# Performance work log

Hardware: AMD Instinct MI355X
Metric: run time of the kernel (lower is better)

Reference implementation:

```python
import jax, jax.numpy as jnp
import numpy as np
from jax import lax

DIM = 64
NUM_EXPERTS = 6
TOP_K = 2
B, H, W = 8, 128, 128
DN = ('NCHW', 'OIHW', 'NCHW')


def setup_inputs() -> dict:
    key = jax.random.key(0)
    ks = jax.random.split(key, 8)
    s_in = 1.0 / np.sqrt(DIM * 9)
    s_r = 1.0 / np.sqrt(DIM)
    return {
        'x': jax.random.normal(ks[0], (B, DIM, H, W), jnp.float32),
        'router_w': jax.random.normal(ks[1], (NUM_EXPERTS, DIM), jnp.float32) * s_r,
        'router_b': jnp.zeros((NUM_EXPERTS,), jnp.float32),
        'expert_bias': jnp.zeros((NUM_EXPERTS,), jnp.float32),
        'w1': jax.random.normal(ks[2], (NUM_EXPERTS, DIM, DIM, 3, 3), jnp.float32) * s_in,
        'b1': jnp.zeros((NUM_EXPERTS, DIM), jnp.float32),
        'w2': jax.random.normal(ks[3], (NUM_EXPERTS, DIM, DIM, 3, 3), jnp.float32) * s_in,
        'b2': jnp.zeros((NUM_EXPERTS, DIM), jnp.float32),
    }


def reference(x, router_w, router_b, expert_bias, w1, b1, w2, b2):
    # ---- router: global avg pool -> linear -> clamp -> +bias -> softmax ----
    pooled = x.mean(axis=(2, 3))                               # [B, C]
    logits = pooled @ router_w.T + router_b                    # [B, E]
    logits = jnp.clip(logits, -10.0, 10.0) + expert_bias[None, :]
    probs = jnp.clip(jax.nn.softmax(logits, axis=1), 1e-6, 1.0)
    top_v, top_i = lax.top_k(probs, TOP_K)                     # [B, K]
    top_v = top_v / (top_v.sum(axis=1, keepdims=True) + 1e-8)
    # per-sample combine weight for each expert: sum of top-k probs routed to it
    w_be = (jax.nn.one_hot(top_i, NUM_EXPERTS, dtype=x.dtype) * top_v[..., None]).sum(axis=1)  # [B, E]

    # ---- experts: Conv3x3 -> GELU -> Conv3x3, vmapped over expert dim ----
    def expert(w1e, b1e, w2e, b2e):
        h = lax.conv_general_dilated(x, w1e, (1, 1), 'SAME', dimension_numbers=DN)
        h = jax.nn.gelu(h + b1e[None, :, None, None])
        h = lax.conv_general_dilated(h, w2e, (1, 1), 'SAME', dimension_numbers=DN)
        return h + b2e[None, :, None, None]

    ys = jax.vmap(expert)(w1, b1, w2, b2)                      # [E, B, C, H, W]
    out = jnp.einsum('be,ebchw->bchw', w_be, ys)
    return out, jnp.zeros((), x.dtype)
```

## Files before the change

### kernel.cpp

```cpp
#include <hip/hip_runtime.h>
#include <hip/hip_bf16.h>
#include <cstdint>

typedef __attribute__((ext_vector_type(8))) short sh8;
typedef __attribute__((ext_vector_type(16))) float f32x16;
typedef unsigned short ushort_t;

#define HH 128
#define WW 128
#define HWSZ (HH*WW)
#define PW 130
#define PW64 (PW*64)
#define IMGSZ ((size_t)PW*PW*64)
#define WBEXP 36864

#define TR 8
#define SROWS 10
#define SCOLS 34
#define ASTR (SCOLS*128)
#define ACHUNKS (SROWS*SCOLS*8)

__device__ __forceinline__ float gelu_tanh(float x) {
    float u = 0.7978845608028654f * (x + 0.044715f * x * x * x);
    return 0.5f * x * (1.0f + tanhf(u));
}
__device__ __forceinline__ ushort_t f2b(float f) {
    __hip_bfloat16 h = __float2bfloat16(f);
    return *reinterpret_cast<ushort_t*>(&h);
}
__device__ __forceinline__ f32x16 mfma_bf16(sh8 a, sh8 b, f32x16 c) {
    return __builtin_amdgcn_mfma_f32_32x32x16_bf16(a, b, c, 0, 0, 0);
}

__device__ __forceinline__ void stage_tile(const ushort_t* __restrict__ imgRow,
                                           char* smem, int w0, int tid) {
#pragma unroll
    for (int it = 0; it < 11; ++it) {
        int idx = tid + it * 256;
        if (idx < ACHUNKS) {
            int row = idx / (SCOLS * 8);
            int rem = idx - row * (SCOLS * 8);
            int col = rem >> 3, ch = rem & 7;
            uint4 v = *reinterpret_cast<const uint4*>(
                imgRow + (size_t)row * PW64 + (size_t)(w0 + col) * 64 + ch * 8);
            int byt = row * ASTR + ((col * 128 + ch * 16) ^ ((col & 7) << 4));
            *reinterpret_cast<uint4*>(smem + byt) = v;
        }
    }
}

__global__ __launch_bounds__(64) void router_kernel(const float* __restrict__ pooled,
                                                    const float* __restrict__ rw,
                                                    const float* __restrict__ rb,
                                                    const float* __restrict__ eb,
                                                    const float* __restrict__ b2,
                                                    int* __restrict__ topi,
                                                    float* __restrict__ topw,
                                                    float* __restrict__ bsum,
                                                    float* __restrict__ outz) {
    __shared__ int sti[16];
    __shared__ float stw[16];
    int b = threadIdx.x;
    if (b == 8) outz[(size_t)8 * 64 * HWSZ] = 0.f;
    if (b < 8) {
        float lg[6];
        for (int e = 0; e < 6; ++e) {
            float s = 0.f;
            for (int c = 0; c < 64; ++c) s += pooled[b * 64 + c] * rw[e * 64 + c];
            s = s * (1.0f / (float)HWSZ) + rb[e];
            lg[e] = fminf(fmaxf(s, -10.f), 10.f) + eb[e];
        }
        float m = lg[0];
        for (int e = 1; e < 6; ++e) m = fmaxf(m, lg[e]);
        float den = 0.f, pr[6];
        for (int e = 0; e < 6; ++e) { pr[e] = expf(lg[e] - m); den += pr[e]; }
        float inv = 1.0f / den;
        for (int e = 0; e < 6; ++e) pr[e] = fminf(fmaxf(pr[e] * inv, 1e-6f), 1.0f);
        int i0 = 0; float v0 = pr[0];
        for (int e = 1; e < 6; ++e) if (pr[e] > v0) { v0 = pr[e]; i0 = e; }
        int i1 = -1; float v1 = -1.f;
        for (int e = 0; e < 6; ++e) { if (e == i0) continue; if (pr[e] > v1) { v1 = pr[e]; i1 = e; } }
        float s2 = v0 + v1 + 1e-8f;
        topi[b * 2 + 0] = i0; topi[b * 2 + 1] = i1;
        topw[b * 2 + 0] = v0 / s2; topw[b * 2 + 1] = v1 / s2;
        sti[b * 2 + 0] = i0; sti[b * 2 + 1] = i1;
        stw[b * 2 + 0] = v0 / s2; stw[b * 2 + 1] = v1 / s2;
    }
    __syncthreads();
    for (int i = threadIdx.x; i < 512; i += 64) {
        int bb = i >> 6, c = i & 63;
        bsum[i] = stw[bb * 2] * b2[sti[bb * 2] * 64 + c] +
                  stw[bb * 2 + 1] * b2[sti[bb * 2 + 1] * 64 + c];
    }
}

__global__ __launch_bounds__(256) void convx_kernel(const float* __restrict__ x,
                                                    ushort_t* __restrict__ xp,
                                                    float* __restrict__ pooled) {
    __shared__ ushort_t lt[128][72];
    int b = blockIdx.x >> 7, h = blockIdx.x & 127;
    int tid = threadIdx.x;
#pragma unroll
    for (int k = 0; k < 8; ++k) {
        int idx = tid + k * 256;
        int ci = idx >> 5, wg = idx & 31;
        float4 v = *reinterpret_cast<const float4*>(
            x + ((size_t)b * 64 + ci) * HWSZ + (size_t)h * WW + wg * 4);
        lt[wg * 4 + 0][ci] = f2b(v.x);
        lt[wg * 4 + 1][ci] = f2b(v.y);
        lt[wg * 4 + 2][ci] = f2b(v.z);
        lt[wg * 4 + 3][ci] = f2b(v.w);
        float s4 = (v.x + v.y) + (v.z + v.w);
#pragma unroll
        for (int m = 16; m > 0; m >>= 1) s4 += __shfl_xor(s4, m, 64);
        if ((tid & 31) == 0) atomicAdd(pooled + b * 64 + ci, s4);
    }
    __syncthreads();
    int w = tid >> 1, half = tid & 1;
    const int4* src = reinterpret_cast<const int4*>(&lt[w][half * 32]);
    int4 a0 = src[0], a1 = src[1], a2 = src[2], a3 = src[3];
    int4* dst = reinterpret_cast<int4*>(
        xp + (((size_t)b * PW + (h + 1)) * PW + (w + 1)) * 64 + half * 32);
    dst[0] = a0; dst[1] = a1; dst[2] = a2; dst[3] = a3;
}

__global__ __launch_bounds__(256) void convw1_kernel(const float* __restrict__ w1,
                                                     ushort_t* __restrict__ wb1f) {
    int blk = blockIdx.x;
    int e = blk / 9, t = blk - e * 9;
    for (int idx = threadIdx.x; idx < 4096; idx += 256) {
        int kc = idx >> 10, n = (idx >> 9) & 1, l = (idx >> 3) & 63, j = idx & 7;
        int co = n * 32 + (l & 31);
        int ci = kc * 16 + (l >> 5) * 8 + j;
        wb1f[(size_t)e * WBEXP + t * 4096 + idx] =
            f2b(w1[(((size_t)e * 64 + co) * 64 + ci) * 9 + t]);
    }
}

__global__ __launch_bounds__(256) void convw2_kernel(const float* __restrict__ w2,
                                                     const int* __restrict__ topi,
                                                     const float* __restrict__ topw,
                                                     ushort_t* __restrict__ wb2f) {
    int blk = blockIdx.x;
    int bs = blk / 9, t = blk - bs * 9;
    int e = topi[bs];
    float cw = topw[bs];
    for (int idx = threadIdx.x; idx < 4096; idx += 256) {
        int kc = idx >> 10, n = (idx >> 9) & 1, l = (idx >> 3) & 63, j = idx & 7;
        int co = n * 32 + (l & 31);
        int ci = kc * 16 + (l >> 5) * 8 + j;
        wb2f[(size_t)bs * WBEXP + t * 4096 + idx] =
            f2b(cw * w2[(((size_t)e * 64 + co) * 64 + ci) * 9 + t]);
    }
}

__global__ __launch_bounds__(256) void halo_kernel(ushort_t* __restrict__ xp,
                                                   ushort_t* __restrict__ hp) {
    int img = blockIdx.x;
    ushort_t* p = (img < 8) ? (xp + (size_t)img * IMGSZ) : (hp + (size_t)(img - 8) * IMGSZ);
    int tid = threadIdx.x;
    int4 z = make_int4(0, 0, 0, 0);
    for (int i = tid; i < 1040; i += 256) {
        reinterpret_cast<int4*>(p)[i] = z;
        reinterpret_cast<int4*>(p + (size_t)129 * PW64)[i] = z;
    }
    for (int i = tid; i < 128 * 8; i += 256) {
        int row = 1 + (i >> 3), j = i & 7;
        reinterpret_cast<int4*>(p + (size_t)row * PW64)[j] = z;
        reinterpret_cast<int4*>(p + ((size_t)row * PW + 129) * 64)[j] = z;
    }
}

__global__ __launch_bounds__(256) void conv1_mfma(const ushort_t* __restrict__ xp,
                                                  const ushort_t* __restrict__ wb1f,
                                                  const float* __restrict__ b1,
                                                  const int* __restrict__ topi,
                                                  ushort_t* __restrict__ hp,
                                                  int nslots, int slot0) {
    __shared__ uint4 smem4[ACHUNKS];
    char* smem = (char*)smem4;
    const int z = blockIdx.z;
    const int b = z / nslots, sl = z - b * nslots, s = slot0 + sl;
    const int e = topi[b * 2 + s];
    const int tid = threadIdx.x, l = tid & 63, wid = tid >> 6;
    const int l31 = l & 31, lh = l >> 5;
    const int ht = blockIdx.x >> 2, wt = blockIdx.x & 3;
    const int h0 = ht * TR, w0 = wt * 32;
    const int r0 = wid * 2;

    stage_tile(xp + (size_t)b * IMGSZ + (size_t)h0 * PW64, smem, w0, tid);
    __syncthreads();

    const ushort_t* wB = wb1f + (size_t)e * WBEXP + l * 8;
    f32x16 acc00, acc01, acc10, acc11;
#pragma unroll
    for (int k2 = 0; k2 < 16; ++k2) { acc00[k2] = 0.f; acc01[k2] = 0.f; acc10[k2] = 0.f; acc11[k2] = 0.f; }

#pragma unroll
    for (int dr = 0; dr < 3; ++dr) {
#pragma unroll
        for (int dc = 0; dc < 3; ++dc) {
            const int t = dr * 3 + dc;
            const int col = dc + l31;
            const int swz = (col & 7) << 4;
#pragma unroll
            for (int kc = 0; kc < 4; ++kc) {
                const int cb = (col * 128 + kc * 32 + lh * 16) ^ swz;
                sh8 a0 = *reinterpret_cast<const sh8*>(smem + (r0 + dr) * ASTR + cb);
                sh8 a1 = *reinterpret_cast<const sh8*>(smem + (r0 + dr + 1) * ASTR + cb);
                sh8 b0 = *reinterpret_cast<const sh8*>(wB + (t * 4 + kc) * 1024);
                sh8 b1 = *reinterpret_cast<const sh8*>(wB + (t * 4 + kc) * 1024 + 512);
                acc00 = mfma_bf16(a0, b0, acc00);
                acc01 = mfma_bf16(a0, b1, acc01);
                acc10 = mfma_bf16(a1, b0, acc10);
                acc11 = mfma_bf16(a1, b1, acc11);
            }
        }
    }

    const float bv0 = b1[e * 64 + l31];
    const float bv1 = b1[e * 64 + 32 + l31];
    const size_t base =
        (((size_t)(sl * 8 + b) * PW + (h0 + r0 + 1)) * PW + (w0 + 1)) * 64 + l31;
#pragma unroll
    for (int i = 0; i < 2; ++i) {
#pragma unroll
        for (int n = 0; n < 2; ++n) {
            f32x16 a = (i == 0) ? (n == 0 ? acc00 : acc01) : (n == 0 ? acc10 : acc11);
            const float bv = n ? bv1 : bv0;
            const size_t ob = base + (size_t)i * PW64 + n * 32;
#pragma unroll
            for (int r = 0; r < 16; ++r) {
                int px = (r & 3) + 8 * (r >> 2) + 4 * lh;
                hp[ob + (size_t)px * 64] = f2b(gelu_tanh(a[r] + bv));
            }
        }
    }
}

template <int NS>
__global__ __launch_bounds__(256) void conv2_mfma(const ushort_t* __restrict__ hp,
                                                  const ushort_t* __restrict__ wb2f,
                                                  const float* __restrict__ bsum,
                                                  float* __restrict__ outF,
                                                  int s0, int addmode) {
    __shared__ uint4 smem4[ACHUNKS];
    char* smem = (char*)smem4;
    const int b = blockIdx.z;
    const int tid = threadIdx.x, l = tid & 63, wid = tid >> 6;
    const int l31 = l & 31, lh = l >> 5;
    const int ht = blockIdx.x >> 2, wt = blockIdx.x & 3;
    const int h0 = ht * TR, w0 = wt * 32;
    const int r0 = wid * 2;

    f32x16 acc00, acc01, acc10, acc11;
#pragma unroll
    for (int k2 = 0; k2 < 16; ++k2) { acc00[k2] = 0.f; acc01[k2] = 0.f; acc10[k2] = 0.f; acc11[k2] = 0.f; }

    for (int si = 0; si < NS; ++si) {
        __syncthreads();
        stage_tile(hp + (size_t)(si * 8 + b) * IMGSZ + (size_t)h0 * PW64, smem, w0, tid);
        __syncthreads();

        const ushort_t* wB = wb2f + (size_t)(b * 2 + s0 + si) * WBEXP + l * 8;
#pragma unroll
        for (int dr = 0; dr < 3; ++dr) {
#pragma unroll
            for (int dc = 0; dc < 3; ++dc) {
                const int t = dr * 3 + dc;
                const int col = dc + l31;
                const int swz = (col & 7) << 4;
#pragma unroll
                for (int kc = 0; kc < 4; ++kc) {
                    const int cb = (col * 128 + kc * 32 + lh * 16) ^ swz;
                    sh8 a0 = *reinterpret_cast<const sh8*>(smem + (r0 + dr) * ASTR + cb);
                    sh8 a1 = *reinterpret_cast<const sh8*>(smem + (r0 + dr + 1) * ASTR + cb);
                    sh8 b0 = *reinterpret_cast<const sh8*>(wB + (t * 4 + kc) * 1024);
                    sh8 b1 = *reinterpret_cast<const sh8*>(wB + (t * 4 + kc) * 1024 + 512);
                    acc00 = mfma_bf16(a0, b0, acc00);
                    acc01 = mfma_bf16(a0, b1, acc01);
                    acc10 = mfma_bf16(a1, b0, acc10);
                    acc11 = mfma_bf16(a1, b1, acc11);
                }
            }
        }
    }

    __syncthreads();
    float* lt = (float*)smem4;
    const float bq0 = addmode ? 0.f : bsum[b * 64 + l31];
    const float bq1 = addmode ? 0.f : bsum[b * 64 + 32 + l31];
#pragma unroll
    for (int i = 0; i < 2; ++i) {
        const int h = h0 + r0 + i;
#pragma unroll
        for (int n = 0; n < 2; ++n) {
            f32x16 a = (i == 0) ? (n == 0 ? acc00 : acc01) : (n == 0 ? acc10 : acc11);
            const float bq = n ? bq1 : bq0;
#pragma unroll
            for (int r = 0; r < 16; ++r) {
                int px = (r & 3) + 8 * (r >> 2) + 4 * lh;
                lt[wid * 1056 + px * 33 + l31] = a[r] + bq;
            }
            const int q = lh, co = l31;
            const size_t ob = ((size_t)(b * 64 + n * 32 + co)) * HWSZ +
                              (size_t)h * WW + w0 + q * 16;
#pragma unroll
            for (int v = 0; v < 4; ++v) {
                float o0 = lt[wid * 1056 + (q * 16 + v * 4 + 0) * 33 + co];
                float o1 = lt[wid * 1056 + (q * 16 + v * 4 + 1) * 33 + co];
                float o2 = lt[wid * 1056 + (q * 16 + v * 4 + 2) * 33 + co];
                float o3 = lt[wid * 1056 + (q * 16 + v * 4 + 3) * 33 + co];
                float4* dst = reinterpret_cast<float4*>(outF + ob + v * 4);
                if (addmode) {
                    float4 pv = *dst;
                    o0 += pv.x; o1 += pv.y; o2 += pv.z; o3 += pv.w;
                }
                float4 o; o.x = o0; o.y = o1; o.z = o2; o.w = o3;
                *dst = o;
            }
        }
    }
}

extern "C" void kernel_launch(void* const* d_in, const int* in_sizes, int n_in,
                              void* d_out, int out_size, void* d_ws, size_t ws_size,
                              hipStream_t stream) {
    const float* x  = (const float*)d_in[0];
    const float* rw = (const float*)d_in[1];
    const float* rb = (const float*)d_in[2];
    const float* eb = (const float*)d_in[3];
    const float* w1 = (const float*)d_in[4];
    const float* b1 = (const float*)d_in[5];
    const float* w2 = (const float*)d_in[6];
    const float* b2 = (const float*)d_in[7];
    float* out = (float*)d_out;

    char* ws = (char*)d_ws;
    float*    pooled = (float*)(ws + 0);
    int*      topi   = (int*)(ws + 2048);
    float*    topw   = (float*)(ws + 2112);
    float*    bsum   = (float*)(ws + 2176);
    ushort_t* wb1f   = (ushort_t*)(ws + 4352);
    ushort_t* wb2f   = (ushort_t*)(ws + 446720);
    ushort_t* xp     = (ushort_t*)(ws + 1626368);
    ushort_t* hp     = (ushort_t*)(ws + 18931968);

    const bool two = ws_size >= 53543168ull;

    hipMemsetAsync(pooled, 0, 512 * sizeof(float), stream);
    hipLaunchKernelGGL(convx_kernel, dim3(1024), dim3(256), 0, stream, x, xp, pooled);
    hipLaunchKernelGGL(router_kernel, dim3(1), dim3(64), 0, stream,
                       pooled, rw, rb, eb, b2, topi, topw, bsum, out);
    hipLaunchKernelGGL(convw1_kernel, dim3(54), dim3(256), 0, stream, w1, wb1f);
    hipLaunchKernelGGL(convw2_kernel, dim3(144), dim3(256), 0, stream, w2, topi, topw, wb2f);
    hipLaunchKernelGGL(halo_kernel, dim3(two ? 24 : 16), dim3(256), 0, stream, xp, hp);

    if (two) {
        hipLaunchKernelGGL(conv1_mfma, dim3(64, 1, 16), dim3(256), 0, stream,
                           xp, wb1f, b1, topi, hp, 2, 0);
        hipLaunchKernelGGL((conv2_mfma<2>), dim3(64, 1, 8), dim3(256), 0, stream,
                           hp, wb2f, bsum, out, 0, 0);
    } else {
        hipLaunchKernelGGL(conv1_mfma, dim3(64, 1, 8), dim3(256), 0, stream,
                           xp, wb1f, b1, topi, hp, 1, 0);
        hipLaunchKernelGGL((conv2_mfma<1>), dim3(64, 1, 8), dim3(256), 0, stream,
                           hp, wb2f, bsum, out, 0, 0);
        hipLaunchKernelGGL(conv1_mfma, dim3(64, 1, 8), dim3(256), 0, stream,
                           xp, wb1f, b1, topi, hp, 1, 1);
        hipLaunchKernelGGL((conv2_mfma<1>), dim3(64, 1, 8), dim3(256), 0, stream,
                           hp, wb2f, bsum, out, 1, 1);
    }
}
```

Measured before the change: 251.7 us.

## Use direct global-to-LDS loads, merge prep kernels, retile conv2 with double-buffered slots

Tile staging switches to global_load_lds, which copies straight into shared memory without going through registers, and moves the XOR swizzle onto the source address. The three weight-convert and halo kernels become one prep kernel to cut launch overhead. Conv1's epilogue writes packed bf16 vectors instead of scalar stores. Conv2 now uses 4-row tiles on a grid of twice as many blocks and prefetches the second slot's tile into a separate buffer while the first is computed. The risks are lower arithmetic intensity per conv2 block and more dependence on compiler scheduling around the sched_barrier hints.

Result: faster. 213.6 us (-15.2%).

```diff
diff --git a/kernel.cpp b/kernel.cpp
--- a/kernel.cpp
+++ b/kernel.cpp
@@ -14,11 +14,17 @@
 #define IMGSZ ((size_t)PW*PW*64)
 #define WBEXP 36864
 
-#define TR 8
-#define SROWS 10
 #define SCOLS 34
-#define ASTR (SCOLS*128)
-#define ACHUNKS (SROWS*SCOLS*8)
+#define ROWB (SCOLS*128)
+#define TR1 8
+#define SR1 10
+#define CH1 (SR1*SCOLS*8)
+#define TR2 4
+#define SR2 6
+#define CH2 (SR2*SCOLS*8)
+
+typedef __attribute__((address_space(1))) const void gvoid_t;
+typedef __attribute__((address_space(3))) void lvoid_t;
 
 __device__ __forceinline__ float gelu_tanh(float x) {
     float u = 0.7978845608028654f * (x + 0.044715f * x * x * x);
@@ -28,23 +34,27 @@
     __hip_bfloat16 h = __float2bfloat16(f);
     return *reinterpret_cast<ushort_t*>(&h);
 }
+__device__ __forceinline__ unsigned pack2(float a, float b) {
+    return (unsigned)f2b(a) | ((unsigned)f2b(b) << 16);
+}
 __device__ __forceinline__ f32x16 mfma_bf16(sh8 a, sh8 b, f32x16 c) {
     return __builtin_amdgcn_mfma_f32_32x32x16_bf16(a, b, c, 0, 0, 0);
 }
 
-__device__ __forceinline__ void stage_tile(const ushort_t* __restrict__ imgRow,
-                                           char* smem, int w0, int tid) {
-#pragma unroll
-    for (int it = 0; it < 11; ++it) {
+template <int NCH>
+__device__ __forceinline__ void stage_gll(const ushort_t* __restrict__ imgRow,
+                                          char* smem, int w0, int tid) {
+#pragma unroll
+    for (int it = 0; it < (NCH + 255) / 256; ++it) {
         int idx = tid + it * 256;
-        if (idx < ACHUNKS) {
+        if ((NCH & 255) == 0 || idx < NCH) {
             int row = idx / (SCOLS * 8);
             int rem = idx - row * (SCOLS * 8);
-            int col = rem >> 3, ch = rem & 7;
-            uint4 v = *reinterpret_cast<const uint4*>(
-                imgRow + (size_t)row * PW64 + (size_t)(w0 + col) * 64 + ch * 8);
-            int byt = row * ASTR + ((col * 128 + ch * 16) ^ ((col & 7) << 4));
-            *reinterpret_cast<uint4*>(smem + byt) = v;
+            int col = rem >> 3;
+            int ch  = (rem & 7) ^ (col & 7);
+            const ushort_t* src = imgRow + (size_t)row * PW64 + (size_t)(w0 + col) * 64 + ch * 8;
+            __builtin_amdgcn_global_load_lds((gvoid_t*)src, (lvoid_t*)(smem + idx * 16),
+                                             16, 0, 0);
         }
     }
 }
@@ -124,50 +134,71 @@
     dst[0] = a0; dst[1] = a1; dst[2] = a2; dst[3] = a3;
 }
 
-__global__ __launch_bounds__(256) void convw1_kernel(const float* __restrict__ w1,
-                                                     ushort_t* __restrict__ wb1f) {
+__global__ __launch_bounds__(256) void prep_kernel(const float* __restrict__ w1,
+                                                   const float* __restrict__ w2,
+                                                   const int* __restrict__ topi,
+                                                   const float* __restrict__ topw,
+                                                   ushort_t* __restrict__ wb1f,
+                                                   ushort_t* __restrict__ wb2f,
+                                                   ushort_t* __restrict__ xp,
+                                                   ushort_t* __restrict__ hp) {
     int blk = blockIdx.x;
-    int e = blk / 9, t = blk - e * 9;
-    for (int idx = threadIdx.x; idx < 4096; idx += 256) {
-        int kc = idx >> 10, n = (idx >> 9) & 1, l = (idx >> 3) & 63, j = idx & 7;
-        int co = n * 32 + (l & 31);
-        int ci = kc * 16 + (l >> 5) * 8 + j;
-        wb1f[(size_t)e * WBEXP + t * 4096 + idx] =
-            f2b(w1[(((size_t)e * 64 + co) * 64 + ci) * 9 + t]);
-    }
-}
-
-__global__ __launch_bounds__(256) void convw2_kernel(const float* __restrict__ w2,
-                                                     const int* __restrict__ topi,
-                                                     const float* __restrict__ topw,
-                                                     ushort_t* __restrict__ wb2f) {
-    int blk = blockIdx.x;
-    int bs = blk / 9, t = blk - bs * 9;
-    int e = topi[bs];
-    float cw = topw[bs];
-    for (int idx = threadIdx.x; idx < 4096; idx += 256) {
-        int kc = idx >> 10, n = (idx >> 9) & 1, l = (idx >> 3) & 63, j = idx & 7;
-        int co = n * 32 + (l & 31);
-        int ci = kc * 16 + (l >> 5) * 8 + j;
-        wb2f[(size_t)bs * WBEXP + t * 4096 + idx] =
-            f2b(cw * w2[(((size_t)e * 64 + co) * 64 + ci) * 9 + t]);
-    }
-}
-
-__global__ __launch_bounds__(256) void halo_kernel(ushort_t* __restrict__ xp,
-                                                   ushort_t* __restrict__ hp) {
-    int img = blockIdx.x;
-    ushort_t* p = (img < 8) ? (xp + (size_t)img * IMGSZ) : (hp + (size_t)(img - 8) * IMGSZ);
     int tid = threadIdx.x;
-    int4 z = make_int4(0, 0, 0, 0);
-    for (int i = tid; i < 1040; i += 256) {
-        reinterpret_cast<int4*>(p)[i] = z;
-        reinterpret_cast<int4*>(p + (size_t)129 * PW64)[i] = z;
-    }
-    for (int i = tid; i < 128 * 8; i += 256) {
-        int row = 1 + (i >> 3), j = i & 7;
-        reinterpret_cast<int4*>(p + (size_t)row * PW64)[j] = z;
-        reinterpret_cast<int4*>(p + ((size_t)row * PW + 129) * 64)[j] = z;
+    if (blk < 54) {
+        int e = blk / 9, t = blk - e * 9;
+        for (int idx = tid; idx < 4096; idx += 256) {
+            int kc = idx >> 10, n = (idx >> 9) & 1, l = (idx >> 3) & 63, j = idx & 7;
+            int co = n * 32 + (l & 31);
+            int ci = kc * 16 + (l >> 5) * 8 + j;
+            wb1f[(size_t)e * WBEXP + t * 4096 + idx] =
+                f2b(w1[(((size_t)e * 64 + co) * 64 + ci) * 9 + t]);
+        }
+    } else if (blk < 198) {
+        int q = blk - 54;
+        int bs = q / 9, t = q - bs * 9;
+        int e = topi[bs];
+        float cw = topw[bs];
+        for (int idx = tid; idx < 4096; idx += 256) {
+            int kc = idx >> 10, n = (idx >> 9) & 1, l = (idx >> 3) & 63, j = idx & 7;
+            int co = n * 32 + (l & 31);
+            int ci = kc * 16 + (l >> 5) * 8 + j;
+            wb2f[(size_t)bs * WBEXP + t * 4096 + idx] =
+                f2b(cw * w2[(((size_t)e * 64 + co) * 64 + ci) * 9 + t]);
+        }
+    } else {
+        int img = blk - 198;
+        ushort_t* p = (img < 8) ? (xp + (size_t)img * IMGSZ)
+                                : (hp + (size_t)(img - 8) * IMGSZ);
+        int4 z = make_int4(0, 0, 0, 0);
+        for (int i = tid; i < 1040; i += 256) {
+            reinterpret_cast<int4*>(p)[i] = z;
+            reinterpret_cast<int4*>(p + (size_t)129 * PW64)[i] = z;
+        }
+        for (int i = tid; i < 128 * 8; i += 256) {
+            int row = 1 + (i >> 3), j = i & 7;
+            reinterpret_cast<int4*>(p + (size_t)row * PW64)[j] = z;
+            reinterpret_cast<int4*>(p + ((size_t)row * PW + 129) * 64)[j] = z;
+        }
+    }
+}
+
+__device__ __forceinline__ void conv_phase1(const char* sm, const ushort_t* wt_,
+                                            int row, int l31, int lh,
+                                            f32x16& acc0, f32x16& acc1, int dc) {
+    sh8 wf[8];
+#pragma unroll
+    for (int kc = 0; kc < 4; ++kc) {
+        wf[kc * 2]     = *reinterpret_cast<const sh8*>(wt_ + kc * 1024);
+        wf[kc * 2 + 1] = *reinterpret_cast<const sh8*>(wt_ + kc * 1024 + 512);
+    }
+    __builtin_amdgcn_sched_barrier(0);
+    const int colb = (dc + l31) * 128;
+    const int swz = ((dc + l31) & 7) << 4;
+#pragma unroll
+    for (int kc = 0; kc < 4; ++kc) {
+        sh8 a = *reinterpret_cast<const sh8*>(sm + row * ROWB + ((colb + (kc * 2 + lh) * 16) ^ swz));
+        acc0 = mfma_bf16(wf[kc * 2], a, acc0);
+        acc1 = mfma_bf16(wf[kc * 2 + 1], a, acc1);
     }
 }
 
@@ -177,62 +208,72 @@
                                                   const int* __restrict__ topi,
                                                   ushort_t* __restrict__ hp,
                                                   int nslots, int slot0) {
-    __shared__ uint4 smem4[ACHUNKS];
-    char* smem = (char*)smem4;
+    __shared__ char smem[CH1 * 16];
     const int z = blockIdx.z;
     const int b = z / nslots, sl = z - b * nslots, s = slot0 + sl;
     const int e = topi[b * 2 + s];
     const int tid = threadIdx.x, l = tid & 63, wid = tid >> 6;
     const int l31 = l & 31, lh = l >> 5;
     const int ht = blockIdx.x >> 2, wt = blockIdx.x & 3;
-    const int h0 = ht * TR, w0 = wt * 32;
+    const int h0 = ht * TR1, w0 = wt * 32;
     const int r0 = wid * 2;
 
-    stage_tile(xp + (size_t)b * IMGSZ + (size_t)h0 * PW64, smem, w0, tid);
-    __syncthreads();
+    stage_gll<CH1>(xp + (size_t)b * IMGSZ + (size_t)h0 * PW64, smem, w0, tid);
 
     const ushort_t* wB = wb1f + (size_t)e * WBEXP + l * 8;
     f32x16 acc00, acc01, acc10, acc11;
 #pragma unroll
     for (int k2 = 0; k2 < 16; ++k2) { acc00[k2] = 0.f; acc01[k2] = 0.f; acc10[k2] = 0.f; acc11[k2] = 0.f; }
+    __syncthreads();
 
 #pragma unroll
     for (int dr = 0; dr < 3; ++dr) {
 #pragma unroll
         for (int dc = 0; dc < 3; ++dc) {
-            const int t = dr * 3 + dc;
-            const int col = dc + l31;
-            const int swz = (col & 7) << 4;
+            const ushort_t* wt_ = wB + (dr * 3 + dc) * 4096;
+            sh8 wf[8];
 #pragma unroll
             for (int kc = 0; kc < 4; ++kc) {
-                const int cb = (col * 128 + kc * 32 + lh * 16) ^ swz;
-                sh8 a0 = *reinterpret_cast<const sh8*>(smem + (r0 + dr) * ASTR + cb);
-                sh8 a1 = *reinterpret_cast<const sh8*>(smem + (r0 + dr + 1) * ASTR + cb);
-                sh8 b0 = *reinterpret_cast<const sh8*>(wB + (t * 4 + kc) * 1024);
-                sh8 b1 = *reinterpret_cast<const sh8*>(wB + (t * 4 + kc) * 1024 + 512);
-                acc00 = mfma_bf16(a0, b0, acc00);
-                acc01 = mfma_bf16(a0, b1, acc01);
-                acc10 = mfma_bf16(a1, b0, acc10);
-                acc11 = mfma_bf16(a1, b1, acc11);
+                wf[kc * 2]     = *reinterpret_cast<const sh8*>(wt_ + kc * 1024);
+                wf[kc * 2 + 1] = *reinterpret_cast<const sh8*>(wt_ + kc * 1024 + 512);
             }
-        }
-    }
-
-    const float bv0 = b1[e * 64 + l31];
-    const float bv1 = b1[e * 64 + 32 + l31];
-    const size_t base =
-        (((size_t)(sl * 8 + b) * PW + (h0 + r0 + 1)) * PW + (w0 + 1)) * 64 + l31;
+            __builtin_amdgcn_sched_barrier(0);
+            const int colb = (dc + l31) * 128;
+            const int swz = ((dc + l31) & 7) << 4;
+#pragma unroll
+            for (int kc = 0; kc < 4; ++kc) {
+                const int cb = (colb + (kc * 2 + lh) * 16) ^ swz;
+                sh8 a0 = *reinterpret_cast<const sh8*>(smem + (r0 + dr) * ROWB + cb);
+                sh8 a1 = *reinterpret_cast<const sh8*>(smem + (r0 + dr + 1) * ROWB + cb);
+                acc00 = mfma_bf16(wf[kc * 2], a0, acc00);
+                acc01 = mfma_bf16(wf[kc * 2 + 1], a0, acc01);
+                acc10 = mfma_bf16(wf[kc * 2], a1, acc10);
+                acc11 = mfma_bf16(wf[kc * 2 + 1], a1, acc11);
+            }
+        }
+    }
+
+    float4 bq[2][4];
+#pragma unroll
+    for (int n = 0; n < 2; ++n)
+#pragma unroll
+        for (int g = 0; g < 4; ++g)
+            bq[n][g] = *reinterpret_cast<const float4*>(b1 + e * 64 + n * 32 + g * 8 + 4 * lh);
+    const size_t pbase = (size_t)(sl * 8 + b) * IMGSZ +
+                         (size_t)(h0 + r0 + 1) * PW64 + (size_t)(w0 + l31 + 1) * 64;
 #pragma unroll
     for (int i = 0; i < 2; ++i) {
 #pragma unroll
         for (int n = 0; n < 2; ++n) {
             f32x16 a = (i == 0) ? (n == 0 ? acc00 : acc01) : (n == 0 ? acc10 : acc11);
-            const float bv = n ? bv1 : bv0;
-            const size_t ob = base + (size_t)i * PW64 + n * 32;
-#pragma unroll
-            for (int r = 0; r < 16; ++r) {
-                int px = (r & 3) + 8 * (r >> 2) + 4 * lh;
-                hp[ob + (size_t)px * 64] = f2b(gelu_tanh(a[r] + bv));
+#pragma unroll
+            for (int g = 0; g < 4; ++g) {
+                float v0 = gelu_tanh(a[g * 4 + 0] + bq[n][g].x);
+                float v1 = gelu_tanh(a[g * 4 + 1] + bq[n][g].y);
+                float v2 = gelu_tanh(a[g * 4 + 2] + bq[n][g].z);
+                float v3 = gelu_tanh(a[g * 4 + 3] + bq[n][g].w);
+                uint2 u; u.x = pack2(v0, v1); u.y = pack2(v2, v3);
+                *reinterpret_cast<uint2*>(hp + pbase + (size_t)i * PW64 + n * 32 + g * 8 + 4 * lh) = u;
             }
         }
     }
@@ -244,81 +285,77 @@
                                                   const float* __restrict__ bsum,
                                                   float* __restrict__ outF,
                                                   int s0, int addmode) {
-    __shared__ uint4 smem4[ACHUNKS];
-    char* smem = (char*)smem4;
+    __shared__ char smem[2][CH2 * 16];
     const int b = blockIdx.z;
     const int tid = threadIdx.x, l = tid & 63, wid = tid >> 6;
     const int l31 = l & 31, lh = l >> 5;
     const int ht = blockIdx.x >> 2, wt = blockIdx.x & 3;
-    const int h0 = ht * TR, w0 = wt * 32;
-    const int r0 = wid * 2;
-
-    f32x16 acc00, acc01, acc10, acc11;
-#pragma unroll
-    for (int k2 = 0; k2 < 16; ++k2) { acc00[k2] = 0.f; acc01[k2] = 0.f; acc10[k2] = 0.f; acc11[k2] = 0.f; }
-
-    for (int si = 0; si < NS; ++si) {
+    const int h0 = ht * TR2, w0 = wt * 32;
+    const int row0 = wid;
+
+    stage_gll<CH2>(hp + (size_t)b * IMGSZ + (size_t)h0 * PW64, smem[0], w0, tid);
+
+    f32x16 acc0, acc1;
+#pragma unroll
+    for (int k2 = 0; k2 < 16; ++k2) { acc0[k2] = 0.f; acc1[k2] = 0.f; }
+    __syncthreads();
+
+    if (NS == 2)
+        stage_gll<CH2>(hp + (size_t)(8 + b) * IMGSZ + (size_t)h0 * PW64, smem[1], w0, tid);
+
+    {
+        const ushort_t* wB = wb2f + (size_t)(b * 2 + s0) * WBEXP + l * 8;
+#pragma unroll
+        for (int dr = 0; dr < 3; ++dr)
+#pragma unroll
+            for (int dc = 0; dc < 3; ++dc)
+                conv_phase1(smem[0], wB + (dr * 3 + dc) * 4096, row0 + dr, l31, lh, acc0, acc1, dc);
+    }
+    if (NS == 2) {
         __syncthreads();
-        stage_tile(hp + (size_t)(si * 8 + b) * IMGSZ + (size_t)h0 * PW64, smem, w0, tid);
-        __syncthreads();
-
-        const ushort_t* wB = wb2f + (size_t)(b * 2 + s0 + si) * WBEXP + l * 8;
-#pragma unroll
-        for (int dr = 0; dr < 3; ++dr) {
-#pragma unroll
-            for (int dc = 0; dc < 3; ++dc) {
-                const int t = dr * 3 + dc;
-                const int col = dc + l31;
-                const int swz = (col & 7) << 4;
-#pragma unroll
-                for (int kc = 0; kc < 4; ++kc) {
-                    const int cb = (col * 128 + kc * 32 + lh * 16) ^ swz;
-                    sh8 a0 = *reinterpret_cast<const sh8*>(smem + (r0 + dr) * ASTR + cb);
-                    sh8 a1 = *reinterpret_cast<const sh8*>(smem + (r0 + dr + 1) * ASTR + cb);
-                    sh8 b0 = *reinterpret_cast<const sh8*>(wB + (t * 4 + kc) * 1024);
-                    sh8 b1 = *reinterpret_cast<const sh8*>(wB + (t * 4 + kc) * 1024 + 512);
-                    acc00 = mfma_bf16(a0, b0, acc00);
-                    acc01 = mfma_bf16(a0, b1, acc01);
-                    acc10 = mfma_bf16(a1, b0, acc10);
-                    acc11 = mfma_bf16(a1, b1, acc11);
-                }
+        const ushort_t* wB = wb2f + (size_t)(b * 2 + s0 + 1) * WBEXP + l * 8;
+#pragma unroll
+        for (int dr = 0; dr < 3; ++dr)
+#pragma unroll
+            for (int dc = 0; dc < 3; ++dc)
+                conv_phase1(smem[1], wB + (dr * 3 + dc) * 4096, row0 + dr, l31, lh, acc0, acc1, dc);
+    }
+
+    __syncthreads();
+    float* lt = reinterpret_cast<float*>(smem[0]) + wid * 1056;
+    float4 bq[2][4];
+#pragma unroll
+    for (int n = 0; n < 2; ++n)
+#pragma unroll
+        for (int g = 0; g < 4; ++g)
+            bq[n][g] = addmode ? make_float4(0.f, 0.f, 0.f, 0.f)
+                               : *reinterpret_cast<const float4*>(bsum + b * 64 + n * 32 + g * 8 + 4 * lh);
+    const int h = h0 + row0;
+#pragma unroll
+    for (int n = 0; n < 2; ++n) {
+        f32x16 a = n ? acc1 : acc0;
+#pragma unroll
+        for (int r = 0; r < 16; ++r) {
+            int co = (r & 3) + 8 * (r >> 2) + 4 * lh;
+            float bv = (r & 3) == 0 ? bq[n][r >> 2].x : (r & 3) == 1 ? bq[n][r >> 2].y
+                     : (r & 3) == 2 ? bq[n][r >> 2].z : bq[n][r >> 2].w;
+            lt[l31 * 33 + co] = a[r] + bv;
+        }
+        const int q = lh, co = l31;
+        const size_t ob = ((size_t)(b * 64 + n * 32 + co)) * HWSZ + (size_t)h * WW + w0 + q * 16;
+#pragma unroll
+        for (int v = 0; v < 4; ++v) {
+            float o0 = lt[(q * 16 + v * 4 + 0) * 33 + co];
+            float o1 = lt[(q * 16 + v * 4 + 1) * 33 + co];
+            float o2 = lt[(q * 16 + v * 4 + 2) * 33 + co];
+            float o3 = lt[(q * 16 + v * 4 + 3) * 33 + co];
+            float4* dst = reinterpret_cast<float4*>(outF + ob + v * 4);
+            if (addmode) {
+                float4 pv = *dst;
+                o0 += pv.x; o1 += pv.y; o2 += pv.z; o3 += pv.w;
             }
-        }
-    }
-
-    __syncthreads();
-    float* lt = (float*)smem4;
-    const float bq0 = addmode ? 0.f : bsum[b * 64 + l31];
-    const float bq1 = addmode ? 0.f : bsum[b * 64 + 32 + l31];
-#pragma unroll
-    for (int i = 0; i < 2; ++i) {
-        const int h = h0 + r0 + i;
-#pragma unroll
-        for (int n = 0; n < 2; ++n) {
-            f32x16 a = (i == 0) ? (n == 0 ? acc00 : acc01) : (n == 0 ? acc10 : acc11);
-            const float bq = n ? bq1 : bq0;
-#pragma unroll
-            for (int r = 0; r < 16; ++r) {
-                int px = (r & 3) + 8 * (r >> 2) + 4 * lh;
-                lt[wid * 1056 + px * 33 + l31] = a[r] + bq;
-            }
-            const int q = lh, co = l31;
-            const size_t ob = ((size_t)(b * 64 + n * 32 + co)) * HWSZ +
-                              (size_t)h * WW + w0 + q * 16;
-#pragma unroll
-            for (int v = 0; v < 4; ++v) {
-                float o0 = lt[wid * 1056 + (q * 16 + v * 4 + 0) * 33 + co];
-                float o1 = lt[wid * 1056 + (q * 16 + v * 4 + 1) * 33 + co];
-                float o2 = lt[wid * 1056 + (q * 16 + v * 4 + 2) * 33 + co];
-                float o3 = lt[wid * 1056 + (q * 16 + v * 4 + 3) * 33 + co];
-                float4* dst = reinterpret_cast<float4*>(outF + ob + v * 4);
-                if (addmode) {
-                    float4 pv = *dst;
-                    o0 += pv.x; o1 += pv.y; o2 += pv.z; o3 += pv.w;
-                }
-                float4 o; o.x = o0; o.y = o1; o.z = o2; o.w = o3;
-                *dst = o;
-            }
+            float4 o; o.x = o0; o.y = o1; o.z = o2; o.w = o3;
+            *dst = o;
         }
     }
 }
@@ -352,23 +389,22 @@
     hipLaunchKernelGGL(convx_kernel, dim3(1024), dim3(256), 0, stream, x, xp, pooled);
     hipLaunchKernelGGL(router_kernel, dim3(1), dim3(64), 0, stream,
                        pooled, rw, rb, eb, b2, topi, topw, bsum, out);
-    hipLaunchKernelGGL(convw1_kernel, dim3(54), dim3(256), 0, stream, w1, wb1f);
-    hipLaunchKernelGGL(convw2_kernel, dim3(144), dim3(256), 0, stream, w2, topi, topw, wb2f);
-    hipLaunchKernelGGL(halo_kernel, dim3(two ? 24 : 16), dim3(256), 0, stream, xp, hp);
+    hipLaunchKernelGGL(prep_kernel, dim3(198 + 8 + (two ? 16 : 8)), dim3(256), 0, stream,
+                       w1, w2, topi, topw, wb1f, wb2f, xp, hp);
 
     if (two) {
         hipLaunchKernelGGL(conv1_mfma, dim3(64, 1, 16), dim3(256), 0, stream,
                            xp, wb1f, b1, topi, hp, 2, 0);
-        hipLaunchKernelGGL((conv2_mfma<2>), dim3(64, 1, 8), dim3(256), 0, stream,
+        hipLaunchKernelGGL((conv2_mfma<2>), dim3(128, 1, 8), dim3(256), 0, stream,
                            hp, wb2f, bsum, out, 0, 0);
     } else {
         hipLaunchKernelGGL(conv1_mfma, dim3(64, 1, 8), dim3(256), 0, stream,
                            xp, wb1f, b1, topi, hp, 1, 0);
-        hipLaunchKernelGGL((conv2_mfma<1>), dim3(64, 1, 8), dim3(256), 0, stream,
+        hipLaunchKernelGGL((conv2_mfma<1>), dim3(128, 1, 8), dim3(256), 0, stream,
                            hp, wb2f, bsum, out, 0, 0);
         hipLaunchKernelGGL(conv1_mfma, dim3(64, 1, 8), dim3(256), 0, stream,
                            xp, wb1f, b1, topi, hp, 1, 1);
-        hipLaunchKernelGGL((conv2_mfma<1>), dim3(64, 1, 8), dim3(256), 0, stream,
+        hipLaunchKernelGGL((conv2_mfma<1>), dim3(128, 1, 8), dim3(256), 0, stream,
                            hp, wb2f, bsum, out, 1, 1);
     }
 }
```
